# Kernel optimization log

Hardware: AMD Instinct MI355X
Metric: run time of the kernel (lower is better)

Reference implementation:

```python
import jax, jax.numpy as jnp
import numpy as np
import math


def pos_enc_3d(h, w, d, c):
    # Faithful PositionalEncoding3D: channels = ceil(c/6)*2 (made even), sin/cos per axis.
    cpe = int(np.ceil(c / 6) * 2)
    if cpe % 2:
        cpe += 1
    inv_freq = 1.0 / (10000.0 ** (np.arange(0, cpe, 2, dtype=np.float32) / cpe))

    def axis_emb(n):
        s = np.arange(n, dtype=np.float32)[:, None] * inv_freq  # (n, cpe//2)
        return np.concatenate([np.sin(s), np.cos(s)], axis=-1)  # (n, cpe)

    ex = np.broadcast_to(axis_emb(h)[:, None, None, :], (h, w, d, cpe))
    ey = np.broadcast_to(axis_emb(w)[None, :, None, :], (h, w, d, cpe))
    ez = np.broadcast_to(axis_emb(d)[None, None, :, :], (h, w, d, cpe))
    emb = np.concatenate([ex, ey, ez], axis=-1)[..., :c]  # (h,w,d,c)
    return jnp.asarray(np.transpose(emb, (3, 0, 1, 2)))  # (c,h,w,d)


def conv3d(x, w, b):
    # x: (b,c,h,w,d), w: (o,i,3,3,3), padding=1
    y = jax.lax.conv_general_dilated(
        x, w, window_strides=(1, 1, 1), padding=[(1, 1)] * 3,
        dimension_numbers=('NCHWD', 'OIHWD', 'NCHWD'))
    return y + b[None, :, None, None, None]


def setup_inputs() -> dict:
    key = jax.random.key(0)
    ks = jax.random.split(key, 12)
    B, C, H, W, D = 2, 64, 16, 16, 16
    C8 = C // 8
    s_emb = 1.0 / math.sqrt(C)
    s_conv = 1.0 / math.sqrt(C * 27)
    return {
        'x': jax.random.normal(ks[0], (B, C, H, W, D), dtype=jnp.float32),
        'Wq': jax.random.normal(ks[1], (C, C), dtype=jnp.float32) * s_emb,
        'Wk': jax.random.normal(ks[2], (C, C), dtype=jnp.float32) * s_emb,
        'Wv': jax.random.normal(ks[3], (C, C), dtype=jnp.float32) * s_emb,
        'qw': jax.random.normal(ks[4], (C8, C, 3, 3, 3), dtype=jnp.float32) * s_conv,
        'qb': jax.random.normal(ks[5], (C8,), dtype=jnp.float32) * 0.01,
        'kw': jax.random.normal(ks[6], (C8, C, 3, 3, 3), dtype=jnp.float32) * s_conv,
        'kb': jax.random.normal(ks[7], (C8,), dtype=jnp.float32) * 0.01,
        'vw': jax.random.normal(ks[8], (C, C, 3, 3, 3), dtype=jnp.float32) * s_conv,
        'vb': jax.random.normal(ks[9], (C,), dtype=jnp.float32) * 0.01,
        'lam1': jax.random.normal(ks[10], (1,), dtype=jnp.float32) * 0.5,
        'lam2': jax.random.normal(ks[11], (1,), dtype=jnp.float32) * 0.5,
    }


def reference(x, Wq, Wk, Wv, qw, qb, kw, kb, vw, vb, lam1, lam2):
    b, c, h, w, d = x.shape
    n = h * w * d
    # NOTE: torch code does `x += pe` in-place inside SelfAttention, so the
    # PE-added x is also what GSA and the residual see.
    pe = pos_enc_3d(h, w, d, c)  # (c,h,w,d)
    x_pe = x + pe[None]

    # ---- SelfAttention (TSA) ----
    tok = x_pe.reshape(b, c, n).transpose(0, 2, 1)  # (b,n,c)
    Q = jnp.einsum('bnc,cd->bnd', tok, Wq)
    K = jnp.einsum('bnc,cd->bnd', tok, Wk)
    V = jnp.einsum('bnc,cd->bnd', tok, Wv)
    A = jax.nn.softmax(jnp.einsum('bic,bjc->bij', Q, K) / math.sqrt(c), axis=-1)
    tsa = jnp.einsum('bij,bjc->bic', A, V).transpose(0, 2, 1).reshape(b, c, h, w, d)

    # ---- GlobalSpatialAttention (GSA) ----
    M = conv3d(x_pe, qw, qb).reshape(b, c // 8, n)   # (b,c/8,n)
    Nk = conv3d(x_pe, kw, kb).reshape(b, c // 8, n)  # (b,c/8,n)
    Wv_ = conv3d(x_pe, vw, vb).reshape(b, c, n)      # (b,c,n)
    Bm = jax.nn.softmax(jnp.einsum('bci,bcj->bij', M, Nk), axis=-1)  # (b,n,n)
    gsa = jnp.einsum('bcj,bij->bci', Wv_, Bm).reshape(b, c, h, w, d)

    return lam1[0] * tsa + lam2[0] * gsa + x_pe
```

## Files before the change

### kernel.cpp

```cpp
#include <hip/hip_runtime.h>
#include <math.h>

#define BB 2
#define CC 64
#define NN 4096
#define CN (CC*NN)
#define NJ 8
#define NT ((NN/NJ)/64)

#define LOG2E 1.4426950408889634f
#define QSCALE 0.18033688011112042f

#define XT_ROWS 4097
#define WQKV_OFF (27*80*64)

typedef __attribute__((ext_vector_type(8))) short short8;
typedef __attribute__((ext_vector_type(4))) float float4v;
typedef unsigned short ushortT;

__device__ __forceinline__ ushortT f2bf(float x) {
    union { float f; unsigned u; } v; v.f = x;
    unsigned r = v.u + 0x7FFF + ((v.u >> 16) & 1);
    return (ushortT)(r >> 16);
}
__device__ __forceinline__ float bf2f(short s) {
    union { unsigned u; float f; } v;
    v.u = ((unsigned)(unsigned short)s) << 16;
    return v.f;
}
__device__ __forceinline__ unsigned pk2(float a, float b) {
    unsigned ua = __float_as_uint(a) + 0x8000u;
    unsigned ub = __float_as_uint(b) + 0x8000u;
    return __builtin_amdgcn_perm(ub, ua, 0x07060302);
}

__device__ __forceinline__ float pe_tab_val(int c, int pos) {
    int c2 = (c < 22) ? c : (c < 44) ? (c - 22) : (c - 44);
    int is_cos = (c2 >= 11);
    int k = c2 - (is_cos ? 11 : 0);
    float freq = exp2f(-1.2079738526863135f * (float)k);
    float arg = (float)pos * freq;
    return is_cos ? cosf(arg) : sinf(arg);
}

__global__ __launch_bounds__(256) void k_pre(const float* __restrict__ x,
                                             const float* __restrict__ qw,
                                             const float* __restrict__ kw,
                                             const float* __restrict__ vw,
                                             const float* __restrict__ Wq,
                                             const float* __restrict__ Wk,
                                             const float* __restrict__ Wv,
                                             float* __restrict__ xpe,
                                             ushortT* __restrict__ Xt,
                                             ushortT* __restrict__ Wr) {
    int blk = blockIdx.x, t = threadIdx.x;
    if (blk < 256) {
        __shared__ float sPE[64][17];
        __shared__ float sT[64][33];
        int b = blk >> 7, pos0 = (blk & 127) * 32;
        #pragma unroll
        for (int k = 0; k < 4; k++) {
            int e = t + k * 256;
            int c = e >> 4, coord = e & 15;
            sPE[c][coord] = pe_tab_val(c, coord);
        }
        __syncthreads();
        int pin = t & 31, cg = t >> 5;
        #pragma unroll
        for (int pass = 0; pass < 8; pass++) {
            int c = pass * 8 + cg;
            int pos = pos0 + pin;
            int coord = (c < 22) ? (pos >> 8) : (c < 44) ? ((pos >> 4) & 15) : (pos & 15);
            size_t gi = (size_t)(b * 64 + c) * NN + pos;
            float v = x[gi] + sPE[c][coord];
            xpe[gi] = v;
            sT[c][pin] = v;
        }
        __syncthreads();
        int icn = t & 63, pg = t >> 6;
        #pragma unroll
        for (int pass = 0; pass < 8; pass++) {
            int po = pass * 4 + pg;
            Xt[((size_t)b * XT_ROWS + pos0 + po + 1) * 64 + icn] = f2bf(sT[icn][po]);
        }
        if ((blk & 127) == 0 && t < 64)
            Xt[((size_t)b * XT_ROWS) * 64 + t] = 0;
    } else {
        int idx = (blk - 256) * 256 + t;
        if (idx < WQKV_OFF) {
            int ic = idx & 63;
            int oc = (idx >> 6) % 80;
            int tap = idx / 5120;
            float v;
            if (oc < 8)       v = qw[(oc * 64 + ic) * 27 + tap] * LOG2E;
            else if (oc < 16) v = kw[((oc - 8) * 64 + ic) * 27 + tap];
            else              v = vw[((oc - 16) * 64 + ic) * 27 + tap];
            Wr[idx] = f2bf(v);
        } else if (idx < WQKV_OFF + 3 * 64 * 64) {
            int idx2 = idx - WQKV_OFF;
            int c = idx2 & 63, d = (idx2 >> 6) & 63, mat = idx2 >> 12;
            const float* Wm = (mat == 0) ? Wq : (mat == 1) ? Wk : Wv;
            float v = Wm[c * 64 + d] * ((mat == 0) ? QSCALE : 1.f);
            Wr[idx] = f2bf(v);
        }
    }
}

__global__ __launch_bounds__(256) void k_qkv(const ushortT* __restrict__ Xt,
                                             const ushortT* __restrict__ Wr,
                                             ushortT* __restrict__ Qb,
                                             ushortT* __restrict__ Kb,
                                             ushortT* __restrict__ Vtb) {
    __shared__ ushortT sVt[64][72];
    int t = threadIdx.x, w = t >> 6, l = t & 63;
    int lane15 = l & 15, q = l >> 4;
    int mat = blockIdx.y, b = blockIdx.z;
    int i0 = blockIdx.x * 64 + w * 16;

    const ushortT* Wt = Wr + WQKV_OFF + mat * 4096;
    const ushortT* xrow = Xt + ((size_t)b * XT_ROWS + i0 + lane15 + 1) * 64;
    short8 a0 = *(const short8*)(xrow + q * 8);
    short8 a1 = *(const short8*)(xrow + 32 + q * 8);
    float4v acc[4];
    #pragma unroll
    for (int cg = 0; cg < 4; cg++) {
        const ushortT* wrow = Wt + (cg * 16 + lane15) * 64;
        short8 b0 = *(const short8*)(wrow + q * 8);
        short8 b1 = *(const short8*)(wrow + 32 + q * 8);
        float4v a = (float4v)0.f;
        a = __builtin_amdgcn_mfma_f32_16x16x32_bf16(a0, b0, a, 0, 0, 0);
        a = __builtin_amdgcn_mfma_f32_16x16x32_bf16(a1, b1, a, 0, 0, 0);
        acc[cg] = a;
    }
    if (mat < 2) {
        ushortT* o = (mat == 0) ? Qb : Kb;
        #pragma unroll
        for (int cg = 0; cg < 4; cg++)
            #pragma unroll
            for (int r = 0; r < 4; r++)
                o[((size_t)(b * NN + i0 + q * 4 + r)) * 64 + cg * 16 + lane15] = f2bf(acc[cg][r]);
    } else {
        int il = w * 16 + q * 4;
        #pragma unroll
        for (int cg = 0; cg < 4; cg++)
            #pragma unroll
            for (int r = 0; r < 4; r++)
                sVt[cg * 16 + lane15][il + r] = f2bf(acc[cg][r]);
        __syncthreads();
        int c2 = t >> 2, seg = t & 3;
        short8 v0 = *(const short8*)&sVt[c2][seg * 16];
        short8 v1 = *(const short8*)&sVt[c2][seg * 16 + 8];
        size_t base = ((size_t)(b * 64 + c2)) * NN + blockIdx.x * 64 + seg * 16;
        *(short8*)(Vtb + base) = v0;
        *(short8*)(Vtb + base + 8) = v1;
    }
}

template<int IS_TSA>
__device__ __forceinline__ void stage_load(short8* kst, short8* vst,
                                           const ushortT* __restrict__ Km,
                                           const ushortT* __restrict__ Vt,
                                           int b, int jb, int t) {
    if (IS_TSA) {
        #pragma unroll
        for (int ps = 0; ps < 2; ps++) {
            int idx = ps * 256 + t, j = idx >> 3, g = idx & 7;
            kst[ps] = *(const short8*)(Km + ((size_t)(b * NN + jb + j)) * 64 + g * 8);
        }
    } else {
        if (t < 64)
            kst[0] = *(const short8*)(Km + ((size_t)(b * NN + jb + t)) * 8);
    }
    #pragma unroll
    for (int ps = 0; ps < 2; ps++) {
        int idx = ps * 256 + t, c = idx >> 3, gj = idx & 7;
        vst[ps] = *(const short8*)(Vt + ((size_t)(b * 64 + c)) * NN + jb + gj * 8);
    }
}

template<int IS_TSA>
__device__ __forceinline__ void stage_write(const short8* kst, const short8* vst,
                                            ushortT* sK, ushortT* sV, int t) {
    if (IS_TSA) {
        #pragma unroll
        for (int ps = 0; ps < 2; ps++) {
            int idx = ps * 256 + t, j = idx >> 3, g = idx & 7;
            *(short8*)(sK + j * 64 + ((g ^ (j & 7)) * 8)) = kst[ps];
        }
    } else {
        if (t < 64)
            *(short8*)(sK + t * 64 + ((t & 7) * 8)) = kst[0];
    }
    #pragma unroll
    for (int ps = 0; ps < 2; ps++) {
        int idx = ps * 256 + t, c = idx >> 3, gj = idx & 7;
        *(short8*)(sV + c * 64 + ((gj ^ (c & 7)) * 8)) = vst[ps];
    }
}

template<int IS_TSA>
__device__ __forceinline__ void flash_body(int it, int jc, int b, int t,
                                           const ushortT* __restrict__ Qm,
                                           const ushortT* __restrict__ Km,
                                           const ushortT* __restrict__ Vt,
                                           float* __restrict__ pM,
                                           float* __restrict__ pL,
                                           ushortT* __restrict__ pAcc,
                                           ushortT* __restrict__ sKb,
                                           ushortT* __restrict__ sVb,
                                           ushortT* __restrict__ sPall) {
    constexpr int KCH = IS_TSA ? 2 : 1;
    constexpr int DQ  = IS_TSA ? 64 : 8;
    int w = t >> 6, l = t & 63;
    int lane15 = l & 15, q = l >> 4;
    int i0 = it * 64 + w * 16;
    ushortT* myP = sPall + w * (16 * 64);

    short8 qf[KCH];
    {
        const ushortT* qrow = Qm + ((size_t)(b * NN + i0 + lane15)) * DQ;
        if (IS_TSA) {
            qf[0] = *(const short8*)(qrow + q * 8);
            qf[1] = *(const short8*)(qrow + 32 + q * 8);
        } else {
            short8 z = (short8)0;
            if (q == 0) z = *(const short8*)qrow;
            qf[0] = z;
        }
    }

    float m_run = -3e38f, Lacc = 0.f;
    float4v O[4];
    #pragma unroll
    for (int cs = 0; cs < 4; cs++) O[cs] = (float4v)0.f;

    const int jbase0 = jc * (NN / NJ);

    short8 kst[2], vst[2];
    stage_load<IS_TSA>(kst, vst, Km, Vt, b, jbase0, t);
    stage_write<IS_TSA>(kst, vst, sKb, sVb, t);
    __syncthreads();

    for (int jt = 0; jt < NT; jt++) {
        int cur = jt & 1;
        ushortT* cK = sKb + cur * 4096;
        ushortT* cV = sVb + cur * 4096;
        bool more = (jt + 1 < NT);

        if (more) stage_load<IS_TSA>(kst, vst, Km, Vt, b, jbase0 + (jt + 1) * 64, t);

        short8 kf[4][KCH];
        #pragma unroll
        for (int sub = 0; sub < 4; sub++) {
            int jr = sub * 16 + lane15;
            if (IS_TSA) {
                kf[sub][0] = *(const short8*)(cK + jr * 64 + (((0 * 4 + q) ^ (lane15 & 7)) * 8));
                kf[sub][1] = *(const short8*)(cK + jr * 64 + (((1 * 4 + q) ^ (lane15 & 7)) * 8));
            } else {
                short8 z = (short8)0;
                if (q == 0) z = *(const short8*)(cK + jr * 64 + ((lane15 & 7) * 8));
                kf[sub][0] = z;
            }
        }

        float4v s[4];
        #pragma unroll
        for (int sub = 0; sub < 4; sub++) {
            float4v acc = (float4v)0.f;
            #pragma unroll
            for (int kc = 0; kc < KCH; kc++)
                acc = __builtin_amdgcn_mfma_f32_16x16x32_bf16(kf[sub][kc], qf[kc], acc, 0, 0, 0);
            s[sub] = acc;
        }

        short8 va[4], vbf[4];
        #pragma unroll
        for (int sub = 0; sub < 4; sub++) {
            int cr = sub * 16 + lane15;
            va[sub]  = *(const short8*)(cV + cr * 64 + ((q ^ (lane15 & 7)) * 8));
            vbf[sub] = *(const short8*)(cV + cr * 64 + (((4 + q) ^ (lane15 & 7)) * 8));
        }

        float tmax = fmaxf(fmaxf(fmaxf(s[0][0], s[0][1]), fmaxf(s[0][2], s[0][3])),
                           fmaxf(fmaxf(s[1][0], s[1][1]), fmaxf(s[1][2], s[1][3])));
        float tmax2 = fmaxf(fmaxf(fmaxf(s[2][0], s[2][1]), fmaxf(s[2][2], s[2][3])),
                            fmaxf(fmaxf(s[3][0], s[3][1]), fmaxf(s[3][2], s[3][3])));
        tmax = fmaxf(tmax, tmax2);
        tmax = fmaxf(tmax, __shfl_xor(tmax, 16));
        tmax = fmaxf(tmax, __shfl_xor(tmax, 32));
        float mnew = fmaxf(m_run, tmax);

        if (__any(mnew > m_run)) {
            float corr = exp2f(m_run - mnew);
            Lacc *= corr;
            float c0 = __shfl(corr, q * 4 + 0);
            float c1 = __shfl(corr, q * 4 + 1);
            float c2 = __shfl(corr, q * 4 + 2);
            float c3 = __shfl(corr, q * 4 + 3);
            #pragma unroll
            for (int cs = 0; cs < 4; cs++) {
                O[cs][0] *= c0; O[cs][1] *= c1; O[cs][2] *= c2; O[cs][3] *= c3;
            }
        }
        m_run = mnew;

        #pragma unroll
        for (int sub = 0; sub < 4; sub++) {
            float p0 = exp2f(s[sub][0] - mnew);
            float p1 = exp2f(s[sub][1] - mnew);
            float p2 = exp2f(s[sub][2] - mnew);
            float p3 = exp2f(s[sub][3] - mnew);
            Lacc += (p0 + p1) + (p2 + p3);
            unsigned lo = pk2(p0, p1), hi = pk2(p2, p3);
            int g = sub * 2 + (q >> 1);
            unsigned* wp = (unsigned*)(myP + lane15 * 64 + ((g ^ (lane15 & 7)) * 8) + (q & 1) * 4);
            wp[0] = lo; wp[1] = hi;
        }

        short8 pf0 = *(const short8*)(myP + lane15 * 64 + (((0 * 4 + q) ^ (lane15 & 7)) * 8));
        short8 pf1 = *(const short8*)(myP + lane15 * 64 + (((1 * 4 + q) ^ (lane15 & 7)) * 8));

        #pragma unroll
        for (int sub = 0; sub < 4; sub++) {
            O[sub] = __builtin_amdgcn_mfma_f32_16x16x32_bf16(pf0, va[sub], O[sub], 0, 0, 0);
            O[sub] = __builtin_amdgcn_mfma_f32_16x16x32_bf16(pf1, vbf[sub], O[sub], 0, 0, 0);
        }

        if (more)
            stage_write<IS_TSA>(kst, vst, sKb + (cur ^ 1) * 4096, sVb + (cur ^ 1) * 4096, t);
        __syncthreads();
    }

    size_t base = (size_t)(b * NJ + jc) * NN + i0;
    Lacc += __shfl_xor(Lacc, 16);
    Lacc += __shfl_xor(Lacc, 32);
    if (q == 0) {
        pL[base + lane15] = Lacc;
        pM[base + lane15] = m_run;
    }
    #pragma unroll
    for (int cs = 0; cs < 4; cs++)
        #pragma unroll
        for (int r = 0; r < 4; r++)
            pAcc[(base + q * 4 + r) * 64 + cs * 16 + lane15] = f2bf(O[cs][r]);
}

__global__ __launch_bounds__(256, 4) void k_tsacv(const ushortT* __restrict__ Qb,
                                                  const ushortT* __restrict__ Kb,
                                                  const ushortT* __restrict__ Vtb,
                                                  const ushortT* __restrict__ Xt,
                                                  const ushortT* __restrict__ Wr,
                                                  const float* __restrict__ qb,
                                                  const float* __restrict__ kb,
                                                  const float* __restrict__ vb,
                                                  ushortT* __restrict__ Mt,
                                                  ushortT* __restrict__ Nt,
                                                  ushortT* __restrict__ Wvt,
                                                  float* __restrict__ pMt, float* __restrict__ pLt,
                                                  ushortT* __restrict__ pAccT) {
    __shared__ ushortT sm[20480];
    int bx = blockIdx.x, t = threadIdx.x;
    if (bx >= 128) {
        int fb = bx - 128;
        int it = fb & 63, jc = (fb >> 6) & 7, b = fb >> 9;
        flash_body<1>(it, jc, b, t, Qb, Kb, Vtb, pMt, pLt, pAccT,
                      sm, sm + 8192, sm + 16384);
    } else {
        int cv = bx;
        int tile = cv & 63, b = cv >> 6;
        int w = t >> 6, l = t & 63, lane15 = l & 15, q = l >> 4;
        int pos0 = tile * 64 + w * 16;
        const ushortT* xb = Xt + (size_t)b * XT_ROWS * 64;
        int pos = pos0 + lane15;
        int dz = pos & 15, wy = (pos >> 4) & 15, hx = pos >> 8;

        ushortT* sW = sm;

        float4v accA[5], accB[5];
        #pragma unroll
        for (int o = 0; o < 5; o++) { accA[o] = (float4v)0.f; accB[o] = (float4v)0.f; }

        short8 ws[3];
        auto ldW = [&](int tap) {
            #pragma unroll
            for (int c3 = 0; c3 < 3; c3++) {
                int idx = t + c3 * 256;
                if (idx < 640)
                    ws[c3] = *(const short8*)(Wr + (size_t)tap * 5120 + idx * 8);
            }
        };
        auto wrW = [&](ushortT* buf) {
            #pragma unroll
            for (int c3 = 0; c3 < 3; c3++) {
                int idx = t + c3 * 256;
                if (idx < 640) {
                    int row = idx >> 3, g = idx & 7;
                    *(short8*)(buf + row * 64 + ((g ^ (row & 7)) * 8)) = ws[c3];
                }
            }
        };

        ldW(0);
        wrW(sW);
        __syncthreads();

        #pragma unroll
        for (int tap = 0; tap < 27; tap++) {
            const int dh = tap / 9 - 1, dw = (tap / 3) % 3 - 1, dd = tap % 3 - 1;
            const int shift = dh * 256 + dw * 16 + dd;
            ushortT* cW = sW + (tap & 1) * 5120;
            bool more = (tap + 1 < 27);

            if (more) ldW(tap + 1);

            bool ok = ((unsigned)(hx + dh) < 16u) &&
                      ((unsigned)(wy + dw) < 16u) &&
                      ((unsigned)(dz + dd) < 16u);
            int row = ok ? (pos + shift + 1) : 0;
            const ushortT* xrow = xb + (size_t)row * 64 + q * 8;
            short8 b0 = *(const short8*)xrow;
            short8 b1 = *(const short8*)(xrow + 32);

            #pragma unroll
            for (int o = 0; o < 5; o++) {
                int wr2 = o * 16 + lane15;
                short8 a0 = *(const short8*)(cW + wr2 * 64 + ((q ^ (lane15 & 7)) * 8));
                short8 a1 = *(const short8*)(cW + wr2 * 64 + (((4 + q) ^ (lane15 & 7)) * 8));
                accA[o] = __builtin_amdgcn_mfma_f32_16x16x32_bf16(a0, b0, accA[o], 0, 0, 0);
                accB[o] = __builtin_amdgcn_mfma_f32_16x16x32_bf16(a1, b1, accB[o], 0, 0, 0);
            }

            if (more) wrW(sW + ((tap + 1) & 1) * 5120);
            __syncthreads();
        }

        #pragma unroll
        for (int o = 0; o < 5; o++) {
            float4v accT = accA[o] + accB[o];
            if (o == 0) {
                #pragma unroll
                for (int r = 0; r < 4; r++) {
                    int ol = q * 4 + r;
                    float v = accT[r];
                    if (ol < 8)
                        Mt[((size_t)(b * NN + pos)) * 8 + ol] = f2bf(v + qb[ol] * LOG2E);
                    else
                        Nt[((size_t)(b * NN + pos)) * 8 + (ol - 8)] = f2bf(v + kb[ol - 8]);
                }
            } else {
                #pragma unroll
                for (int r = 0; r < 4; r++) {
                    int oc = (o - 1) * 16 + q * 4 + r;
                    Wvt[((size_t)(b * 64 + oc)) * NN + pos] = f2bf(accT[r] + vb[oc]);
                }
            }
        }
    }
}

__global__ __launch_bounds__(256, 4) void k_gsa(const ushortT* __restrict__ Mtb,
                                                const ushortT* __restrict__ Ntb,
                                                const ushortT* __restrict__ Wvtb,
                                                float* __restrict__ pMg, float* __restrict__ pLg,
                                                ushortT* __restrict__ pAccG) {
    __shared__ ushortT sK[2][64 * 64];
    __shared__ ushortT sV[2][64 * 64];
    __shared__ ushortT sP[4][16 * 64];
    int t = threadIdx.x;
    flash_body<0>(blockIdx.x, blockIdx.y, blockIdx.z, t, Mtb, Ntb, Wvtb, pMg, pLg, pAccG,
                  &sK[0][0], &sV[0][0], &sP[0][0]);
}

__device__ __forceinline__ void reduce_set(const float* __restrict__ pM,
                                           const float* __restrict__ pL,
                                           const ushortT* __restrict__ pAcc,
                                           int b, int n, int seg, float* v) {
    float mv[NJ], M = -3e38f;
    #pragma unroll
    for (int jcc = 0; jcc < NJ; jcc++) {
        mv[jcc] = pM[(size_t)(b * NJ + jcc) * NN + n];
        M = fmaxf(M, mv[jcc]);
    }
    float L = 0.f;
    #pragma unroll
    for (int e = 0; e < 8; e++) v[e] = 0.f;
    #pragma unroll
    for (int jcc = 0; jcc < NJ; jcc++) {
        size_t rb = (size_t)(b * NJ + jcc) * NN + n;
        float wgt = exp2f(mv[jcc] - M);
        L += pL[rb] * wgt;
        short8 x0 = *(const short8*)(pAcc + rb * 64 + seg * 8);
        #pragma unroll
        for (int e = 0; e < 8; e++) v[e] += wgt * bf2f(x0[e]);
    }
    float invL = 1.f / L;
    #pragma unroll
    for (int e = 0; e < 8; e++) v[e] *= invL;
}

__global__ __launch_bounds__(256) void k_reduce(const float* __restrict__ pMt,
                                                const float* __restrict__ pLt,
                                                const ushortT* __restrict__ pAccT,
                                                const float* __restrict__ pMg,
                                                const float* __restrict__ pLg,
                                                const ushortT* __restrict__ pAccG,
                                                const float* __restrict__ xpe,
                                                const float* __restrict__ lam1,
                                                const float* __restrict__ lam2,
                                                float* __restrict__ out) {
    __shared__ float sT[32][65];
    __shared__ float sG[32][65];
    int t = threadIdx.x;
    int b = blockIdx.y;
    int n0 = blockIdx.x * 32;
    int pp = t >> 3, seg = t & 7;
    int n = n0 + pp;

    float vt[8], vg[8];
    reduce_set(pMt, pLt, pAccT, b, n, seg, vt);
    reduce_set(pMg, pLg, pAccG, b, n, seg, vg);
    #pragma unroll
    for (int e = 0; e < 8; e++) {
        sT[pp][seg * 8 + e] = vt[e];
        sG[pp][seg * 8 + e] = vg[e];
    }
    __syncthreads();

    int c = t >> 2, ns = (t & 3) * 8;
    float la1 = lam1[0], la2 = lam2[0];
    size_t ob = ((size_t)(b * 64 + c)) * NN + n0 + ns;
    const float* xp = xpe + ob;
    #pragma unroll
    for (int j = 0; j < 8; j += 4) {
        float4 ov;
        ov.x = la1 * sT[ns + j + 0][c] + la2 * sG[ns + j + 0][c] + xp[j + 0];
        ov.y = la1 * sT[ns + j + 1][c] + la2 * sG[ns + j + 1][c] + xp[j + 1];
        ov.z = la1 * sT[ns + j + 2][c] + la2 * sG[ns + j + 2][c] + xp[j + 2];
        ov.w = la1 * sT[ns + j + 3][c] + la2 * sG[ns + j + 3][c] + xp[j + 3];
        *(float4*)(out + ob + j) = ov;
    }
}

extern "C" void kernel_launch(void* const* d_in, const int* in_sizes, int n_in,
                              void* d_out, int out_size, void* d_ws, size_t ws_size,
                              hipStream_t stream) {
    const float* x    = (const float*)d_in[0];
    const float* Wq   = (const float*)d_in[1];
    const float* Wk   = (const float*)d_in[2];
    const float* Wv   = (const float*)d_in[3];
    const float* qw   = (const float*)d_in[4];
    const float* qb   = (const float*)d_in[5];
    const float* kw   = (const float*)d_in[6];
    const float* kb   = (const float*)d_in[7];
    const float* vw   = (const float*)d_in[8];
    const float* vb   = (const float*)d_in[9];
    const float* lam1 = (const float*)d_in[10];
    const float* lam2 = (const float*)d_in[11];
    float* out = (float*)d_out;

    char* W = (char*)d_ws;
    float*   xpe   = (float*)(W);
    ushortT* Qb    = (ushortT*)(W + (2u << 20));
    ushortT* Kb    = (ushortT*)(W + (3u << 20));
    ushortT* Vtb   = (ushortT*)(W + (4u << 20));
    ushortT* Mtb   = (ushortT*)(W + (5u << 20));
    ushortT* Ntb   = (ushortT*)(W + (5u << 20) + (1u << 17));
    ushortT* Wvtb  = (ushortT*)(W + (5u << 20) + (2u << 17));
    ushortT* Xt    = (ushortT*)(W + (6u << 20) + (2u << 17));
    ushortT* Wr    = (ushortT*)(W + (7u << 20) + (1u << 19));
    float*   pLt   = (float*)(W + (8u << 20));
    float*   pLg   = (float*)(W + (8u << 20) + (1u << 18));
    float*   pMt   = (float*)(W + (8u << 20) + (2u << 18));
    float*   pMg   = (float*)(W + (8u << 20) + (3u << 18));
    ushortT* pAccT = (ushortT*)(W + (9u << 20));
    ushortT* pAccG = (ushortT*)(W + (17u << 20));

    k_pre<<<dim3(256 + (WQKV_OFF + 3 * 64 * 64 + 255) / 256), dim3(256), 0, stream>>>(
        x, qw, kw, vw, Wq, Wk, Wv, xpe, Xt, Wr);
    k_qkv<<<dim3(64, 3, BB), dim3(256), 0, stream>>>(Xt, Wr, Qb, Kb, Vtb);
    k_tsacv<<<dim3(128 + 64 * NJ * BB), dim3(256), 0, stream>>>(
        Qb, Kb, Vtb, Xt, Wr, qb, kb, vb, Mtb, Ntb, Wvtb, pMt, pLt, pAccT);
    k_gsa<<<dim3(64, NJ, BB), dim3(256), 0, stream>>>(
        Mtb, Ntb, Wvtb, pMg, pLg, pAccG);
    k_reduce<<<dim3(NN / 32, BB), dim3(256), 0, stream>>>(
        pMt, pLt, pAccT, pMg, pLg, pAccG, xpe, lam1, lam2, out);
}
```

Measured before the change: 136.4 us.

## Process two query sub-tiles per wave to reuse staged K/V tiles

```diff
diff --git a/kernel.cpp b/kernel.cpp
--- a/kernel.cpp
+++ b/kernel.cpp
@@ -213,26 +213,29 @@
     constexpr int DQ  = IS_TSA ? 64 : 8;
     int w = t >> 6, l = t & 63;
     int lane15 = l & 15, q = l >> 4;
-    int i0 = it * 64 + w * 16;
+    int i0a = it * 128 + w * 16;
     ushortT* myP = sPall + w * (16 * 64);
 
-    short8 qf[KCH];
-    {
-        const ushortT* qrow = Qm + ((size_t)(b * NN + i0 + lane15)) * DQ;
+    short8 qf[2][KCH];
+    #pragma unroll
+    for (int si = 0; si < 2; si++) {
+        const ushortT* qrow = Qm + ((size_t)(b * NN + i0a + si * 64 + lane15)) * DQ;
         if (IS_TSA) {
-            qf[0] = *(const short8*)(qrow + q * 8);
-            qf[1] = *(const short8*)(qrow + 32 + q * 8);
+            qf[si][0] = *(const short8*)(qrow + q * 8);
+            qf[si][1] = *(const short8*)(qrow + 32 + q * 8);
         } else {
             short8 z = (short8)0;
             if (q == 0) z = *(const short8*)qrow;
-            qf[0] = z;
-        }
-    }
-
-    float m_run = -3e38f, Lacc = 0.f;
-    float4v O[4];
-    #pragma unroll
-    for (int cs = 0; cs < 4; cs++) O[cs] = (float4v)0.f;
+            qf[si][0] = z;
+        }
+    }
+
+    float m_run[2] = {-3e38f, -3e38f}, Lacc[2] = {0.f, 0.f};
+    float4v O[2][4];
+    #pragma unroll
+    for (int si = 0; si < 2; si++)
+        #pragma unroll
+        for (int cs = 0; cs < 4; cs++) O[si][cs] = (float4v)0.f;
 
     const int jbase0 = jc * (NN / NJ);
 
@@ -263,15 +266,17 @@
             }
         }
 
-        float4v s[4];
-        #pragma unroll
-        for (int sub = 0; sub < 4; sub++) {
-            float4v acc = (float4v)0.f;
-            #pragma unroll
-            for (int kc = 0; kc < KCH; kc++)
-                acc = __builtin_amdgcn_mfma_f32_16x16x32_bf16(kf[sub][kc], qf[kc], acc, 0, 0, 0);
-            s[sub] = acc;
-        }
+        float4v s[2][4];
+        #pragma unroll
+        for (int si = 0; si < 2; si++)
+            #pragma unroll
+            for (int sub = 0; sub < 4; sub++) {
+                float4v acc = (float4v)0.f;
+                #pragma unroll
+                for (int kc = 0; kc < KCH; kc++)
+                    acc = __builtin_amdgcn_mfma_f32_16x16x32_bf16(kf[sub][kc], qf[si][kc], acc, 0, 0, 0);
+                s[si][sub] = acc;
+            }
 
         short8 va[4], vbf[4];
         #pragma unroll
@@ -281,49 +286,53 @@
             vbf[sub] = *(const short8*)(cV + cr * 64 + (((4 + q) ^ (lane15 & 7)) * 8));
         }
 
-        float tmax = fmaxf(fmaxf(fmaxf(s[0][0], s[0][1]), fmaxf(s[0][2], s[0][3])),
-                           fmaxf(fmaxf(s[1][0], s[1][1]), fmaxf(s[1][2], s[1][3])));
-        float tmax2 = fmaxf(fmaxf(fmaxf(s[2][0], s[2][1]), fmaxf(s[2][2], s[2][3])),
-                            fmaxf(fmaxf(s[3][0], s[3][1]), fmaxf(s[3][2], s[3][3])));
-        tmax = fmaxf(tmax, tmax2);
-        tmax = fmaxf(tmax, __shfl_xor(tmax, 16));
-        tmax = fmaxf(tmax, __shfl_xor(tmax, 32));
-        float mnew = fmaxf(m_run, tmax);
-
-        if (__any(mnew > m_run)) {
-            float corr = exp2f(m_run - mnew);
-            Lacc *= corr;
-            float c0 = __shfl(corr, q * 4 + 0);
-            float c1 = __shfl(corr, q * 4 + 1);
-            float c2 = __shfl(corr, q * 4 + 2);
-            float c3 = __shfl(corr, q * 4 + 3);
-            #pragma unroll
-            for (int cs = 0; cs < 4; cs++) {
-                O[cs][0] *= c0; O[cs][1] *= c1; O[cs][2] *= c2; O[cs][3] *= c3;
-            }
-        }
-        m_run = mnew;
-
-        #pragma unroll
-        for (int sub = 0; sub < 4; sub++) {
-            float p0 = exp2f(s[sub][0] - mnew);
-            float p1 = exp2f(s[sub][1] - mnew);
-            float p2 = exp2f(s[sub][2] - mnew);
-            float p3 = exp2f(s[sub][3] - mnew);
-            Lacc += (p0 + p1) + (p2 + p3);
-            unsigned lo = pk2(p0, p1), hi = pk2(p2, p3);
-            int g = sub * 2 + (q >> 1);
-            unsigned* wp = (unsigned*)(myP + lane15 * 64 + ((g ^ (lane15 & 7)) * 8) + (q & 1) * 4);
-            wp[0] = lo; wp[1] = hi;
-        }
-
-        short8 pf0 = *(const short8*)(myP + lane15 * 64 + (((0 * 4 + q) ^ (lane15 & 7)) * 8));
-        short8 pf1 = *(const short8*)(myP + lane15 * 64 + (((1 * 4 + q) ^ (lane15 & 7)) * 8));
-
-        #pragma unroll
-        for (int sub = 0; sub < 4; sub++) {
-            O[sub] = __builtin_amdgcn_mfma_f32_16x16x32_bf16(pf0, va[sub], O[sub], 0, 0, 0);
-            O[sub] = __builtin_amdgcn_mfma_f32_16x16x32_bf16(pf1, vbf[sub], O[sub], 0, 0, 0);
+        #pragma unroll
+        for (int si = 0; si < 2; si++) {
+            float tmax = fmaxf(fmaxf(fmaxf(s[si][0][0], s[si][0][1]), fmaxf(s[si][0][2], s[si][0][3])),
+                               fmaxf(fmaxf(s[si][1][0], s[si][1][1]), fmaxf(s[si][1][2], s[si][1][3])));
+            float tmax2 = fmaxf(fmaxf(fmaxf(s[si][2][0], s[si][2][1]), fmaxf(s[si][2][2], s[si][2][3])),
+                                fmaxf(fmaxf(s[si][3][0], s[si][3][1]), fmaxf(s[si][3][2], s[si][3][3])));
+            tmax = fmaxf(tmax, tmax2);
+            tmax = fmaxf(tmax, __shfl_xor(tmax, 16));
+            tmax = fmaxf(tmax, __shfl_xor(tmax, 32));
+            float mnew = fmaxf(m_run[si], tmax);
+
+            if (__any(mnew > m_run[si])) {
+                float corr = exp2f(m_run[si] - mnew);
+                Lacc[si] *= corr;
+                float c0 = __shfl(corr, q * 4 + 0);
+                float c1 = __shfl(corr, q * 4 + 1);
+                float c2 = __shfl(corr, q * 4 + 2);
+                float c3 = __shfl(corr, q * 4 + 3);
+                #pragma unroll
+                for (int cs = 0; cs < 4; cs++) {
+                    O[si][cs][0] *= c0; O[si][cs][1] *= c1;
+                    O[si][cs][2] *= c2; O[si][cs][3] *= c3;
+                }
+            }
+            m_run[si] = mnew;
+
+            #pragma unroll
+            for (int sub = 0; sub < 4; sub++) {
+                float p0 = exp2f(s[si][sub][0] - mnew);
+                float p1 = exp2f(s[si][sub][1] - mnew);
+                float p2 = exp2f(s[si][sub][2] - mnew);
+                float p3 = exp2f(s[si][sub][3] - mnew);
+                Lacc[si] += (p0 + p1) + (p2 + p3);
+                unsigned lo = pk2(p0, p1), hi = pk2(p2, p3);
+                int g = sub * 2 + (q >> 1);
+                unsigned* wp = (unsigned*)(myP + lane15 * 64 + ((g ^ (lane15 & 7)) * 8) + (q & 1) * 4);
+                wp[0] = lo; wp[1] = hi;
+            }
+
+            short8 pf0 = *(const short8*)(myP + lane15 * 64 + (((0 * 4 + q) ^ (lane15 & 7)) * 8));
+            short8 pf1 = *(const short8*)(myP + lane15 * 64 + (((1 * 4 + q) ^ (lane15 & 7)) * 8));
+
+            #pragma unroll
+            for (int sub = 0; sub < 4; sub++) {
+                O[si][sub] = __builtin_amdgcn_mfma_f32_16x16x32_bf16(pf0, va[sub], O[si][sub], 0, 0, 0);
+                O[si][sub] = __builtin_amdgcn_mfma_f32_16x16x32_bf16(pf1, vbf[sub], O[si][sub], 0, 0, 0);
+            }
         }
 
         if (more)
@@ -331,21 +340,25 @@
         __syncthreads();
     }
 
-    size_t base = (size_t)(b * NJ + jc) * NN + i0;
-    Lacc += __shfl_xor(Lacc, 16);
-    Lacc += __shfl_xor(Lacc, 32);
-    if (q == 0) {
-        pL[base + lane15] = Lacc;
-        pM[base + lane15] = m_run;
-    }
-    #pragma unroll
-    for (int cs = 0; cs < 4; cs++)
-        #pragma unroll
-        for (int r = 0; r < 4; r++)
-            pAcc[(base + q * 4 + r) * 64 + cs * 16 + lane15] = f2bf(O[cs][r]);
-}
-
-__global__ __launch_bounds__(256, 4) void k_tsacv(const ushortT* __restrict__ Qb,
+    #pragma unroll
+    for (int si = 0; si < 2; si++) {
+        size_t base = (size_t)(b * NJ + jc) * NN + i0a + si * 64;
+        float Ls = Lacc[si];
+        Ls += __shfl_xor(Ls, 16);
+        Ls += __shfl_xor(Ls, 32);
+        if (q == 0) {
+            pL[base + lane15] = Ls;
+            pM[base + lane15] = m_run[si];
+        }
+        #pragma unroll
+        for (int cs = 0; cs < 4; cs++)
+            #pragma unroll
+            for (int r = 0; r < 4; r++)
+                pAcc[(base + q * 4 + r) * 64 + cs * 16 + lane15] = f2bf(O[si][cs][r]);
+    }
+}
+
+__global__ __launch_bounds__(256, 3) void k_tsacv(const ushortT* __restrict__ Qb,
                                                   const ushortT* __restrict__ Kb,
                                                   const ushortT* __restrict__ Vtb,
                                                   const ushortT* __restrict__ Xt,
@@ -362,7 +375,7 @@
     int bx = blockIdx.x, t = threadIdx.x;
     if (bx >= 128) {
         int fb = bx - 128;
-        int it = fb & 63, jc = (fb >> 6) & 7, b = fb >> 9;
+        int it = fb & 31, jc = (fb >> 5) & 7, b = fb >> 8;
         flash_body<1>(it, jc, b, t, Qb, Kb, Vtb, pMt, pLt, pAccT,
                       sm, sm + 8192, sm + 16384);
     } else {
@@ -458,7 +471,7 @@
     }
 }
 
-__global__ __launch_bounds__(256, 4) void k_gsa(const ushortT* __restrict__ Mtb,
+__global__ __launch_bounds__(256, 3) void k_gsa(const ushortT* __restrict__ Mtb,
                                                 const ushortT* __restrict__ Ntb,
                                                 const ushortT* __restrict__ Wvtb,
                                                 float* __restrict__ pMg, float* __restrict__ pLg,
@@ -578,9 +591,9 @@
     k_pre<<<dim3(256 + (WQKV_OFF + 3 * 64 * 64 + 255) / 256), dim3(256), 0, stream>>>(
         x, qw, kw, vw, Wq, Wk, Wv, xpe, Xt, Wr);
     k_qkv<<<dim3(64, 3, BB), dim3(256), 0, stream>>>(Xt, Wr, Qb, Kb, Vtb);
-    k_tsacv<<<dim3(128 + 64 * NJ * BB), dim3(256), 0, stream>>>(
+    k_tsacv<<<dim3(128 + 32 * NJ * BB), dim3(256), 0, stream>>>(
         Qb, Kb, Vtb, Xt, Wr, qb, kb, vb, Mtb, Ntb, Wvtb, pMt, pLt, pAccT);
-    k_gsa<<<dim3(64, NJ, BB), dim3(256), 0, stream>>>(
+    k_gsa<<<dim3(32, NJ, BB), dim3(256), 0, stream>>>(
         Mtb, Ntb, Wvtb, pMg, pLg, pAccG);
     k_reduce<<<dim3(NN / 32, BB), dim3(256), 0, stream>>>(
         pMt, pLt, pAccT, pMg, pLg, pAccG, xpe, lam1, lam2, out);
```

Measured after the change: 135.3 us. About the same (-0.8%).
